# Kernel tuning notes

Measured on AMD Instinct MI355X. Metric: run time of the kernel, lower is better.

## Reference

```python
import jax, jax.numpy as jnp
import numpy as np

H = 48; W = 48; WS = 8; NH = 12; FTH = 0.4; EPS = 1e-6


def _layernorm(x, w, b):
    mu = jnp.mean(x, axis=-1, keepdims=True)
    var = jnp.mean((x - mu) ** 2, axis=-1, keepdims=True)
    return (x - mu) * jax.lax.rsqrt(var + EPS) * w + b


def _mha(x, w_qkv, b_qkv, w_o, b_o, key_mask=None):
    # x: (Bn, N, C); w_qkv: (3, C, C); key_mask: (Bn, N) bool or None
    Bn, N, C = x.shape
    d = C // NH
    qkv = jnp.einsum('bnc,tcd->tbnd', x, w_qkv) + b_qkv[:, None, None, :]
    q, k, v = [t.reshape(Bn, N, NH, d).transpose(0, 2, 1, 3) for t in qkv]
    s = jnp.einsum('bhqd,bhkd->bhqk', q, k) / jnp.sqrt(jnp.asarray(d, x.dtype))
    if key_mask is not None:
        s = jnp.where(key_mask[:, None, None, :], s, jnp.asarray(-1e9, s.dtype))
    p = jax.nn.softmax(s, axis=-1)
    ctx = jnp.einsum('bhqk,bhkd->bhqd', p, v).transpose(0, 2, 1, 3).reshape(Bn, N, C)
    return ctx @ w_o + b_o


def _forward(x, mask, w_qkv_g, b_qkv_g, w_o_g, b_o_g, w_qkv_l, b_qkv_l, w_o_l, b_o_l,
             ln1_w, ln1_b, ln2_w, ln2_b, w_fc1, b_fc1, w_fc2, b_fc2):
    B, L, C = x.shape
    shortcut = x
    xn = _layernorm(x, ln1_w, ln1_b)

    # avg_pool2d(mask, 4, 4) -> (B, H, W); fg/bg split
    pooled = mask.reshape(B, 1, H, 4, W, 4).mean(axis=(3, 5))[:, 0]      # (B,H,W)
    fg = pooled > FTH                                                    # bool (B,H,W)
    fg_tok = fg.reshape(B, L)
    bg = (~fg).astype(x.dtype)
    # window-level bg mask: avg_pool(bg, WS) > 0 -> window contains any bg token
    bg_win = bg.reshape(B, H // WS, WS, W // WS, WS).mean(axis=(2, 4)) > 0.0   # (B, nH, nW)
    bg_win_tok = jnp.broadcast_to(bg_win[:, :, None, :, None],
                                  (B, H // WS, WS, W // WS, WS)).reshape(B, L)

    # local windowed attention on all windows (equivalent on bg windows; masked out elsewhere)
    xw = xn.reshape(B, H // WS, WS, W // WS, WS, C).transpose(0, 1, 3, 2, 4, 5)
    xw = xw.reshape(-1, WS * WS, C)                                      # (B*nWin, WS*WS, C)
    lout = _mha(xw, w_qkv_l, b_qkv_l, w_o_l, b_o_l)
    lout = lout.reshape(B, H // WS, W // WS, WS, WS, C).transpose(0, 1, 3, 2, 4, 5)
    lout = lout.reshape(B, L, C)

    # global attention with fg key mask (fg queries attend fg keys only)
    gout = _mha(xn, w_qkv_g, b_qkv_g, w_o_g, b_o_g, key_mask=fg_tok)

    # scatter-back semantics: fg positions take global output; bg-window positions take local output; rest zero
    zero = jnp.zeros((), x.dtype)
    x_new = jnp.where(fg_tok[..., None], gout,
                      jnp.where(bg_win_tok[..., None], lout, zero))

    x1 = shortcut + x_new
    h = _layernorm(x1, ln2_w, ln2_b)
    h = jax.nn.gelu(h @ w_fc1 + b_fc1, approximate=False) @ w_fc2 + b_fc2
    return x1 + h


def setup_inputs() -> dict:
    key = jax.random.key(0)
    ks = jax.random.split(key, 8)
    B, L, C, M = 2, H * W, 768, 3072
    s = 0.02
    return {
        'x': jax.random.normal(ks[0], (B, L, C), jnp.float32),
        'mask': jax.random.uniform(ks[1], (B, 1, 4 * H, 4 * W), jnp.float32),
        'w_qkv_g': jax.random.normal(ks[2], (3, C, C), jnp.float32) * s,
        'b_qkv_g': jnp.zeros((3, C), jnp.float32),
        'w_o_g': jax.random.normal(ks[3], (C, C), jnp.float32) * s,
        'b_o_g': jnp.zeros((C,), jnp.float32),
        'w_qkv_l': jax.random.normal(ks[4], (3, C, C), jnp.float32) * s,
        'b_qkv_l': jnp.zeros((3, C), jnp.float32),
        'w_o_l': jax.random.normal(ks[5], (C, C), jnp.float32) * s,
        'b_o_l': jnp.zeros((C,), jnp.float32),
        'ln1_w': jnp.ones((C,), jnp.float32),
        'ln1_b': jnp.zeros((C,), jnp.float32),
        'ln2_w': jnp.ones((C,), jnp.float32),
        'ln2_b': jnp.zeros((C,), jnp.float32),
        'w_fc1': jax.random.normal(ks[6], (C, M), jnp.float32) * s,
        'b_fc1': jnp.zeros((M,), jnp.float32),
        'w_fc2': jax.random.normal(ks[7], (M, C), jnp.float32) * s,
        'b_fc2': jnp.zeros((C,), jnp.float32),
    }


def reference(x, mask, w_qkv_g, b_qkv_g, w_o_g, b_o_g, w_qkv_l, b_qkv_l, w_o_l, b_o_l,
              ln1_w, ln1_b, ln2_w, ln2_b, w_fc1, b_fc1, w_fc2, b_fc2):
    return _forward(x, mask, w_qkv_g, b_qkv_g, w_o_g, b_o_g, w_qkv_l, b_qkv_l, w_o_l, b_o_l,
                    ln1_w, ln1_b, ln2_w, ln2_b, w_fc1, b_fc1, w_fc2, b_fc2)
```

## Files before the change

kernel.cpp:

```cpp
#include <hip/hip_runtime.h>
#include <math.h>

#define Lh 2304
#define Ch 768
#define NHh 12
#define Bh 2
#define QS 4608

typedef unsigned short ushort_t;
typedef unsigned int uint_t;
typedef __attribute__((ext_vector_type(8))) short bf16x8;
typedef __attribute__((ext_vector_type(4))) float f32x4;
#define MFMA16(a, b, c) __builtin_amdgcn_mfma_f32_16x16x32_bf16(a, b, c, 0, 0, 0)

__device__ __forceinline__ ushort_t f2bf(float f) {
    union { float f; uint_t u; } v; v.f = f;
    uint_t u = v.u + 0x7fffu + ((v.u >> 16) & 1u);
    return (ushort_t)(u >> 16);
}
__device__ __forceinline__ uint_t pack2bf(float a, float b) {
    return (uint_t)f2bf(a) | ((uint_t)f2bf(b) << 16);
}

__device__ __forceinline__ void llds16(ushort_t* dst, const ushort_t* src) {
    __builtin_amdgcn_global_load_lds(
        (__attribute__((address_space(1))) void*)(const_cast<ushort_t*>(src)),
        (__attribute__((address_space(3))) void*)dst, 16, 0, 0);
}

__global__ __launch_bounds__(256)
void layernorm_bf16_kernel(const float* __restrict__ x, const float* __restrict__ w,
                           const float* __restrict__ b, ushort_t* __restrict__ y)
{
    int row = blockIdx.x;
    int tid = threadIdx.x;
    const float* xr = x + (size_t)row * Ch;
    float v0 = xr[tid], v1 = xr[tid + 256], v2 = xr[tid + 512];
    __shared__ float red[256];
    red[tid] = v0 + v1 + v2;
    __syncthreads();
    for (int st = 128; st > 0; st >>= 1) {
        if (tid < st) red[tid] += red[tid + st];
        __syncthreads();
    }
    float mean = red[0] * (1.0f / 768.0f);
    __syncthreads();
    float d0 = v0 - mean, d1 = v1 - mean, d2 = v2 - mean;
    red[tid] = d0 * d0 + d1 * d1 + d2 * d2;
    __syncthreads();
    for (int st = 128; st > 0; st >>= 1) {
        if (tid < st) red[tid] += red[tid + st];
        __syncthreads();
    }
    float rstd = rsqrtf(red[0] * (1.0f / 768.0f) + 1e-6f);
    ushort_t* yr = y + (size_t)row * Ch;
    yr[tid]       = f2bf(d0 * rstd * w[tid]       + b[tid]);
    yr[tid + 256] = f2bf(d1 * rstd * w[tid + 256] + b[tid + 256]);
    yr[tid + 512] = f2bf(d2 * rstd * w[tid + 512] + b[tid + 512]);
}

__global__ __launch_bounds__(64)
void mask_kernel(const float* __restrict__ mask, float* __restrict__ fg,
                 float* __restrict__ bgw)
{
    int win = blockIdx.x;
    int b = win / 36, w = win % 36;
    int wi = w / 6, wj = w % 6;
    int lane = threadIdx.x;
    int i = wi * 8 + (lane >> 3), j = wj * 8 + (lane & 7);
    const float* mb = mask + (size_t)b * 192 * 192 + (size_t)(i * 4) * 192 + j * 4;
    float s = 0.0f;
    #pragma unroll
    for (int di = 0; di < 4; ++di) {
        float4 v = *(const float4*)(mb + (size_t)di * 192);
        s += v.x + v.y + v.z + v.w;
    }
    float f = (s * (1.0f / 16.0f) > 0.4f) ? 1.0f : 0.0f;
    fg[b * Lh + i * 48 + j] = f;
    unsigned long long bg = __ballot(f == 0.0f);
    if (lane == 0) bgw[win] = bg ? 1.0f : 0.0f;
}

__global__ __launch_bounds__(256)
void transpose_all_kernel(const float* __restrict__ w_qkv_g, const float* __restrict__ w_qkv_l,
                          const float* __restrict__ w_o_g, const float* __restrict__ w_o_l,
                          const float* __restrict__ w_fc1, const float* __restrict__ w_fc2,
                          ushort_t* __restrict__ wtq, ushort_t* __restrict__ wt_o_g,
                          ushort_t* __restrict__ wt_o_l, ushort_t* __restrict__ wt_fc1,
                          ushort_t* __restrict__ wt_fc2)
{
    int blk = blockIdx.x;
    const float* W; ushort_t* D; int K, N, nx, bx;
    const size_t CC = (size_t)Ch * Ch;
    if (blk < 432)       { int t = blk / 144; bx = blk % 144;
                           W = w_qkv_g + t * CC; D = wtq + t * CC; K = 768; N = 768; nx = 12; }
    else if (blk < 864)  { int r = blk - 432; int t = r / 144; bx = r % 144;
                           W = w_qkv_l + t * CC; D = wtq + (size_t)2304 * 768 + t * CC;
                           K = 768; N = 768; nx = 12; }
    else if (blk < 1008) { bx = blk - 864;  W = w_o_g; D = wt_o_g; K = 768; N = 768; nx = 12; }
    else if (blk < 1152) { bx = blk - 1008; W = w_o_l; D = wt_o_l; K = 768; N = 768; nx = 12; }
    else if (blk < 1728) { bx = blk - 1152; W = w_fc1; D = wt_fc1; K = 768; N = 3072; nx = 48; }
    else                 { bx = blk - 1728; W = w_fc2; D = wt_fc2; K = 3072; N = 768; nx = 12; }
    int n0 = (bx % nx) * 64;
    int k0 = (bx / nx) * 64;
    int tid = threadIdx.x;
    __shared__ float T[64][65];
    #pragma unroll
    for (int i = 0; i < 16; ++i) {
        int lin = i * 256 + tid;
        int r = lin >> 6, c = lin & 63;
        T[r][c] = W[(size_t)(k0 + r) * N + n0 + c];
    }
    __syncthreads();
    #pragma unroll
    for (int i = 0; i < 4; ++i) {
        int lin = i * 256 + tid;
        int r = lin >> 4, c0 = (lin & 15) * 4;
        uint_t lo = pack2bf(T[c0][r], T[c0 + 1][r]);
        uint_t hi = pack2bf(T[c0 + 2][r], T[c0 + 3][r]);
        *(uint2*)&D[(size_t)(n0 + r) * K + k0 + c0] = make_uint2(lo, hi);
    }
}

template<int BNt>
__global__ __launch_bounds__(256)
void gemm_bf16_t(const ushort_t* __restrict__ A, const ushort_t* __restrict__ Bt,
                 const float* __restrict__ bias, const float* __restrict__ residual,
                 void* __restrict__ C, int M, int N, int K, int flags)
{
    __shared__ ushort_t AsL[2][128 * 32];
    __shared__ ushort_t BsL[2][BNt * 32];
    int bm = blockIdx.y * 128;
    int bn = blockIdx.x * BNt;
    int tid = threadIdx.x;
    int lane = tid & 63;
    int wave = tid >> 6;
    int wm = wave >> 1, wn = wave & 1;
    int quad = lane >> 4, l15 = lane & 15;
    constexpr int NJ = BNt / 32;

    int srow = lane >> 2;
    int sg8 = ((lane & 3) ^ ((lane >> 3) & 3)) * 8;
    int fsw = (l15 >> 1) & 3;

    f32x4 acc[4][NJ];
    #pragma unroll
    for (int i = 0; i < 4; ++i)
        #pragma unroll
        for (int j = 0; j < NJ; ++j)
            acc[i][j] = (f32x4){0.f, 0.f, 0.f, 0.f};

    int iters = K / 32;
    llds16(&AsL[0][wave * 512], A + (size_t)(bm + wave * 16 + srow) * K + sg8);
    llds16(&AsL[0][(wave + 4) * 512], A + (size_t)(bm + (wave + 4) * 16 + srow) * K + sg8);
    llds16(&BsL[0][wave * 512], Bt + (size_t)(bn + wave * 16 + srow) * K + sg8);
    if (BNt == 128)
        llds16(&BsL[0][(wave + 4) * 512], Bt + (size_t)(bn + (wave + 4) * 16 + srow) * K + sg8);

    for (int kt = 0; kt < iters; ++kt) {
        int cur = kt & 1;
        __syncthreads();

        bf16x8 af[4], bfr[NJ];
        #pragma unroll
        for (int i = 0; i < 4; ++i)
            af[i] = *(const bf16x8*)&AsL[cur][(wm * 64 + i * 16 + l15) * 32 + ((quad ^ fsw) * 8)];
        #pragma unroll
        for (int j = 0; j < NJ; ++j)
            bfr[j] = *(const bf16x8*)&BsL[cur][(wn * (BNt / 2) + j * 16 + l15) * 32 + ((quad ^ fsw) * 8)];

        if (kt + 1 < iters) {
            int k0 = (kt + 1) * 32;
            int nxt = 1 - cur;
            llds16(&AsL[nxt][wave * 512], A + (size_t)(bm + wave * 16 + srow) * K + k0 + sg8);
            llds16(&AsL[nxt][(wave + 4) * 512], A + (size_t)(bm + (wave + 4) * 16 + srow) * K + k0 + sg8);
            llds16(&BsL[nxt][wave * 512], Bt + (size_t)(bn + wave * 16 + srow) * K + k0 + sg8);
            if (BNt == 128)
                llds16(&BsL[nxt][(wave + 4) * 512], Bt + (size_t)(bn + (wave + 4) * 16 + srow) * K + k0 + sg8);
        }

        #pragma unroll
        for (int i = 0; i < 4; ++i)
            #pragma unroll
            for (int j = 0; j < NJ; ++j)
                acc[i][j] = MFMA16(bfr[j], af[i], acc[i][j]);
    }

    #pragma unroll
    for (int i = 0; i < 4; ++i) {
        int row = bm + wm * 64 + i * 16 + l15;
        #pragma unroll
        for (int j = 0; j < NJ; ++j) {
            int col = bn + wn * (BNt / 2) + j * 16 + quad * 4;
            float4 bia = *(const float4*)&bias[col];
            float o0 = acc[i][j][0] + bia.x;
            float o1 = acc[i][j][1] + bia.y;
            float o2 = acc[i][j][2] + bia.z;
            float o3 = acc[i][j][3] + bia.w;
            if (flags & 1) {
                o0 = o0 * 0.5f * (1.0f + erff(o0 * 0.70710678f));
                o1 = o1 * 0.5f * (1.0f + erff(o1 * 0.70710678f));
                o2 = o2 * 0.5f * (1.0f + erff(o2 * 0.70710678f));
                o3 = o3 * 0.5f * (1.0f + erff(o3 * 0.70710678f));
            }
            if (residual) {
                float4 rs = *(const float4*)&residual[(size_t)row * N + col];
                o0 += rs.x; o1 += rs.y; o2 += rs.z; o3 += rs.w;
            }
            if (flags & 2) {
                *(uint2*)&((ushort_t*)C)[(size_t)row * N + col] =
                    make_uint2(pack2bf(o0, o1), pack2bf(o2, o3));
            } else {
                *(float4*)&((float*)C)[(size_t)row * N + col] =
                    make_float4(o0, o1, o2, o3);
            }
        }
    }
}

__global__ __launch_bounds__(256)
void oproj_dual_kernel(const ushort_t* __restrict__ ctxg, const ushort_t* __restrict__ ctxl,
                       const ushort_t* __restrict__ Wg, const ushort_t* __restrict__ Wl,
                       const float* __restrict__ biasg, const float* __restrict__ biasl,
                       const float* __restrict__ x, float* __restrict__ x1,
                       const float* __restrict__ fg, const float* __restrict__ bgw)
{
    __shared__ ushort_t AsL[2][128 * 32];
    __shared__ ushort_t BsL[2][64 * 32];
    int bm = blockIdx.y * 128;
    int bn = blockIdx.x * 64;
    int tid = threadIdx.x;
    int lane = tid & 63;
    int wave = tid >> 6;
    int wm = wave >> 1, wn = wave & 1;
    int quad = lane >> 4, l15 = lane & 15;

    int srow = lane >> 2;
    int sg8 = ((lane & 3) ^ ((lane >> 3) & 3)) * 8;
    int fsw = (l15 >> 1) & 3;
    const int K = Ch, N = Ch, iters = Ch / 32;

    f32x4 accg[4][2], accl[4][2];
    #pragma unroll
    for (int i = 0; i < 4; ++i)
        #pragma unroll
        for (int j = 0; j < 2; ++j) {
            accg[i][j] = (f32x4){0.f, 0.f, 0.f, 0.f};
            accl[i][j] = (f32x4){0.f, 0.f, 0.f, 0.f};
        }

    #pragma unroll
    for (int pass = 0; pass < 2; ++pass) {
        const ushort_t* A = pass ? ctxl : ctxg;
        const ushort_t* Bt = pass ? Wl : Wg;
        if (pass) __syncthreads();
        llds16(&AsL[0][wave * 512], A + (size_t)(bm + wave * 16 + srow) * K + sg8);
        llds16(&AsL[0][(wave + 4) * 512], A + (size_t)(bm + (wave + 4) * 16 + srow) * K + sg8);
        llds16(&BsL[0][wave * 512], Bt + (size_t)(bn + wave * 16 + srow) * K + sg8);

        for (int kt = 0; kt < iters; ++kt) {
            int cur = kt & 1;
            __syncthreads();
            bf16x8 af[4], bfr[2];
            #pragma unroll
            for (int i = 0; i < 4; ++i)
                af[i] = *(const bf16x8*)&AsL[cur][(wm * 64 + i * 16 + l15) * 32 + ((quad ^ fsw) * 8)];
            #pragma unroll
            for (int j = 0; j < 2; ++j)
                bfr[j] = *(const bf16x8*)&BsL[cur][(wn * 32 + j * 16 + l15) * 32 + ((quad ^ fsw) * 8)];
            if (kt + 1 < iters) {
                int k0 = (kt + 1) * 32;
                int nxt = 1 - cur;
                llds16(&AsL[nxt][wave * 512], A + (size_t)(bm + wave * 16 + srow) * K + k0 + sg8);
                llds16(&AsL[nxt][(wave + 4) * 512], A + (size_t)(bm + (wave + 4) * 16 + srow) * K + k0 + sg8);
                llds16(&BsL[nxt][wave * 512], Bt + (size_t)(bn + wave * 16 + srow) * K + k0 + sg8);
            }
            if (pass == 0) {
                #pragma unroll
                for (int i = 0; i < 4; ++i)
                    #pragma unroll
                    for (int j = 0; j < 2; ++j)
                        accg[i][j] = MFMA16(bfr[j], af[i], accg[i][j]);
            } else {
                #pragma unroll
                for (int i = 0; i < 4; ++i)
                    #pragma unroll
                    for (int j = 0; j < 2; ++j)
                        accl[i][j] = MFMA16(bfr[j], af[i], accl[i][j]);
            }
        }
    }

    #pragma unroll
    for (int i = 0; i < 4; ++i) {
        int row = bm + wm * 64 + i * 16 + l15;
        int bb = (row >= Lh) ? 1 : 0;
        int n = row - bb * Lh;
        int ii = n / 48, jj = n % 48;
        float keepg = (fg[row] != 0.0f) ? 1.0f : 0.0f;
        float keepl = (keepg == 0.0f &&
                       bgw[bb * 36 + (ii >> 3) * 6 + (jj >> 3)] != 0.0f) ? 1.0f : 0.0f;
        #pragma unroll
        for (int j = 0; j < 2; ++j) {
            int col = bn + wn * 32 + j * 16 + quad * 4;
            float4 bg4 = *(const float4*)&biasg[col];
            float4 bl4 = *(const float4*)&biasl[col];
            float4 x4 = *(const float4*)&x[(size_t)row * N + col];
            float4 o;
            o.x = x4.x + keepg * (accg[i][j][0] + bg4.x) + keepl * (accl[i][j][0] + bl4.x);
            o.y = x4.y + keepg * (accg[i][j][1] + bg4.y) + keepl * (accl[i][j][1] + bl4.y);
            o.z = x4.z + keepg * (accg[i][j][2] + bg4.z) + keepl * (accl[i][j][2] + bl4.z);
            o.w = x4.w + keepg * (accg[i][j][3] + bg4.w) + keepl * (accl[i][j][3] + bl4.w);
            *(float4*)&x1[(size_t)row * N + col] = o;
        }
    }
}

__device__ __forceinline__ void attn_global_body(
    const ushort_t* __restrict__ QKV, const float* __restrict__ fg,
    ushort_t* __restrict__ O, int tile, int h, int b,
    ushort_t (*Ks)[72], ushort_t (*Vt)[72], ushort_t (*Ps)[72], float* fgs)
{
    int tid = threadIdx.x;
    int lane = tid & 63;
    int wave = tid >> 6;
    int quad = lane >> 4, l15 = lane & 15;

    bf16x8 aq[2][2];
    #pragma unroll
    for (int s = 0; s < 2; ++s) {
        int ql = wave * 32 + s * 16 + l15;
        int tok = tile * 128 + ql;
        const ushort_t* qbase = QKV + (size_t)(b * Lh + tok) * QS + h * 64;
        #pragma unroll
        for (int step = 0; step < 2; ++step)
            aq[s][step] = *(const bf16x8*)(qbase + step * 32 + quad * 8);
    }

    float l_part[2] = {0.f, 0.f};
    f32x4 o_acc[2][4];
    #pragma unroll
    for (int s = 0; s < 2; ++s)
        #pragma unroll
        for (int t4 = 0; t4 < 4; ++t4) o_acc[s][t4] = (f32x4){0.f, 0.f, 0.f, 0.f};

    uint4 kx[2], vx[2];
    #pragma unroll
    for (int it = 0; it < 2; ++it) {
        int e = tid + it * 256;
        int row = e >> 3, g = e & 7;
        const ushort_t* base = QKV + (size_t)(b * Lh + row) * QS + h * 64 + g * 8;
        kx[it] = *(const uint4*)(base + 768);
        vx[it] = *(const uint4*)(base + 1536);
    }
    float fgn = 0.f;
    if (tid < 64) fgn = fg[b * Lh + tid];

    for (int kt = 0; kt < 36; ++kt) {
        __syncthreads();
        #pragma unroll
        for (int it = 0; it < 2; ++it) {
            int e = tid + it * 256;
            int row = e >> 3, g = e & 7;
            *(uint4*)&Ks[row][g * 8] = kx[it];
            union { uint4 raw; ushort_t us[8]; } vv;
            vv.raw = vx[it];
            int col = row ^ (g << 3);
            #pragma unroll
            for (int j = 0; j < 8; ++j) Vt[g * 8 + j][col] = vv.us[j];
        }
        if (tid < 64) fgs[tid] = (fgn - 1.0f) * 1e9f;
        __syncthreads();

        if (kt + 1 < 36) {
            #pragma unroll
            for (int it = 0; it < 2; ++it) {
                int e = tid + it * 256;
                int row = e >> 3, g = e & 7;
                int tok = (kt + 1) * 64 + row;
                const ushort_t* base = QKV + (size_t)(b * Lh + tok) * QS + h * 64 + g * 8;
                kx[it] = *(const uint4*)(base + 768);
                vx[it] = *(const uint4*)(base + 1536);
            }
            if (tid < 64) fgn = fg[b * Lh + (kt + 1) * 64 + tid];
        }

        f32x4 s4[2][4];
        #pragma unroll
        for (int s = 0; s < 2; ++s)
            #pragma unroll
            for (int j4 = 0; j4 < 4; ++j4) s4[s][j4] = (f32x4){0.f, 0.f, 0.f, 0.f};
        #pragma unroll
        for (int step = 0; step < 2; ++step) {
            bf16x8 bk[4];
            #pragma unroll
            for (int j4 = 0; j4 < 4; ++j4)
                bk[j4] = *(const bf16x8*)&Ks[j4 * 16 + l15][step * 32 + quad * 8];
            #pragma unroll
            for (int s = 0; s < 2; ++s)
                #pragma unroll
                for (int j4 = 0; j4 < 4; ++j4)
                    s4[s][j4] = MFMA16(bk[j4], aq[s][step], s4[s][j4]);
        }
        #pragma unroll
        for (int s = 0; s < 2; ++s) {
            int p0 = wave * 32 + s * 16;
            #pragma unroll
            for (int j4 = 0; j4 < 4; ++j4) {
                float4 mb4 = *(const float4*)&fgs[j4 * 16 + quad * 4];
                float e0 = __expf(s4[s][j4][0] * 0.125f + mb4.x);
                float e1 = __expf(s4[s][j4][1] * 0.125f + mb4.y);
                float e2 = __expf(s4[s][j4][2] * 0.125f + mb4.z);
                float e3 = __expf(s4[s][j4][3] * 0.125f + mb4.w);
                l_part[s] += (e0 + e1) + (e2 + e3);
                uint_t a01 = __builtin_amdgcn_perm(__float_as_uint(e1), __float_as_uint(e0), 0x07060302u);
                uint_t a23 = __builtin_amdgcn_perm(__float_as_uint(e3), __float_as_uint(e2), 0x07060302u);
                *(uint2*)&Ps[p0 + l15][j4 * 16 + quad * 4] = make_uint2(a01, a23);
            }
        }
        #pragma unroll
        for (int step = 0; step < 2; ++step) {
            bf16x8 bv[4];
            #pragma unroll
            for (int t4 = 0; t4 < 4; ++t4) {
                int dd = t4 * 16 + l15;
                int cb = ((step * 4 + quad) ^ ((dd >> 3) & 7)) * 8;
                bv[t4] = *(const bf16x8*)&Vt[dd][cb];
            }
            #pragma unroll
            for (int s = 0; s < 2; ++s) {
                int p0 = wave * 32 + s * 16;
                bf16x8 a = *(const bf16x8*)&Ps[p0 + l15][step * 32 + quad * 8];
                #pragma unroll
                for (int t4 = 0; t4 < 4; ++t4)
                    o_acc[s][t4] = MFMA16(bv[t4], a, o_acc[s][t4]);
            }
        }
    }

    #pragma unroll
    for (int s = 0; s < 2; ++s) {
        float v = l_part[s];
        v += __shfl_xor(v, 16, 64);
        v += __shfl_xor(v, 32, 64);
        float inv = 1.0f / v;
        int ql = wave * 32 + s * 16 + l15;
        int tok = tile * 128 + ql;
        ushort_t* ob = O + (size_t)(b * Lh + tok) * Ch + h * 64;
        #pragma unroll
        for (int t4 = 0; t4 < 4; ++t4) {
            *(uint2*)&ob[t4 * 16 + quad * 4] =
                make_uint2(pack2bf(o_acc[s][t4][0] * inv, o_acc[s][t4][1] * inv),
                           pack2bf(o_acc[s][t4][2] * inv, o_acc[s][t4][3] * inv));
        }
    }
}

__device__ __forceinline__ void attn_local_body(
    const ushort_t* __restrict__ QKV, ushort_t* __restrict__ O,
    int tile, int h, int b,
    ushort_t (*Ks)[72], ushort_t (*Vt)[72], ushort_t (*Ps)[72])
{
    int tid = threadIdx.x;
    int lane = tid & 63;
    int wave = tid >> 6;
    int quad = lane >> 4, l15 = lane & 15;
    int wi = tile / 6, wj = tile % 6;

    bf16x8 aq[2];
    {
        int ql = wave * 16 + l15;
        int tok = (wi * 8 + (ql >> 3)) * 48 + wj * 8 + (ql & 7);
        const ushort_t* qbase = QKV + (size_t)(b * Lh + tok) * QS + 2304 + h * 64;
        #pragma unroll
        for (int step = 0; step < 2; ++step)
            aq[step] = *(const bf16x8*)(qbase + step * 32 + quad * 8);
    }

    float l_part = 0.f;
    f32x4 o_acc[4];
    #pragma unroll
    for (int t4 = 0; t4 < 4; ++t4) o_acc[t4] = (f32x4){0.f, 0.f, 0.f, 0.f};

    #pragma unroll
    for (int it = 0; it < 2; ++it) {
        int e = tid + it * 256;
        int row = e >> 3, g = e & 7;
        int tok = (wi * 8 + (row >> 3)) * 48 + wj * 8 + (row & 7);
        const ushort_t* base = QKV + (size_t)(b * Lh + tok) * QS + 2304 + h * 64 + g * 8;
        uint4 kvv = *(const uint4*)(base + 768);
        *(uint4*)&Ks[row][g * 8] = kvv;
        union { uint4 raw; ushort_t us[8]; } vv;
        vv.raw = *(const uint4*)(base + 1536);
        int col = row ^ (g << 3);
        #pragma unroll
        for (int j = 0; j < 8; ++j) Vt[g * 8 + j][col] = vv.us[j];
    }
    __syncthreads();

    f32x4 s4[4];
    #pragma unroll
    for (int j4 = 0; j4 < 4; ++j4) s4[j4] = (f32x4){0.f, 0.f, 0.f, 0.f};
    #pragma unroll
    for (int step = 0; step < 2; ++step) {
        bf16x8 bk[4];
        #pragma unroll
        for (int j4 = 0; j4 < 4; ++j4)
            bk[j4] = *(const bf16x8*)&Ks[j4 * 16 + l15][step * 32 + quad * 8];
        #pragma unroll
        for (int j4 = 0; j4 < 4; ++j4)
            s4[j4] = MFMA16(bk[j4], aq[step], s4[j4]);
    }
    int p0 = wave * 16;
    #pragma unroll
    for (int j4 = 0; j4 < 4; ++j4) {
        float e0 = __expf(s4[j4][0] * 0.125f);
        float e1 = __expf(s4[j4][1] * 0.125f);
        float e2 = __expf(s4[j4][2] * 0.125f);
        float e3 = __expf(s4[j4][3] * 0.125f);
        l_part += (e0 + e1) + (e2 + e3);
        uint_t a01 = __builtin_amdgcn_perm(__float_as_uint(e1), __float_as_uint(e0), 0x07060302u);
        uint_t a23 = __builtin_amdgcn_perm(__float_as_uint(e3), __float_as_uint(e2), 0x07060302u);
        *(uint2*)&Ps[p0 + l15][j4 * 16 + quad * 4] = make_uint2(a01, a23);
    }
    #pragma unroll
    for (int step = 0; step < 2; ++step) {
        bf16x8 bv[4];
        #pragma unroll
        for (int t4 = 0; t4 < 4; ++t4) {
            int dd = t4 * 16 + l15;
            int cb = ((step * 4 + quad) ^ ((dd >> 3) & 7)) * 8;
            bv[t4] = *(const bf16x8*)&Vt[dd][cb];
        }
        bf16x8 a = *(const bf16x8*)&Ps[p0 + l15][step * 32 + quad * 8];
        #pragma unroll
        for (int t4 = 0; t4 < 4; ++t4)
            o_acc[t4] = MFMA16(bv[t4], a, o_acc[t4]);
    }

    {
        float v = l_part;
        v += __shfl_xor(v, 16, 64);
        v += __shfl_xor(v, 32, 64);
        float inv = 1.0f / v;
        int ql = wave * 16 + l15;
        int tok = (wi * 8 + (ql >> 3)) * 48 + wj * 8 + (ql & 7);
        ushort_t* ob = O + (size_t)(b * Lh + tok) * Ch + h * 64;
        #pragma unroll
        for (int t4 = 0; t4 < 4; ++t4) {
            *(uint2*)&ob[t4 * 16 + quad * 4] =
                make_uint2(pack2bf(o_acc[t4][0] * inv, o_acc[t4][1] * inv),
                           pack2bf(o_acc[t4][2] * inv, o_acc[t4][3] * inv));
        }
    }
}

__global__ __launch_bounds__(256)
void attn_fused_kernel(const ushort_t* __restrict__ QKV, const float* __restrict__ fg,
                       ushort_t* __restrict__ ctxg, ushort_t* __restrict__ ctxl)
{
    __shared__ ushort_t Ks[64][72];
    __shared__ ushort_t Vt[64][72];
    __shared__ ushort_t Ps[128][72];
    __shared__ float fgs[64];

    int gid = blockIdx.x;
    if (gid < 432) {
        int tile = gid % 18;
        int h = (gid / 18) % NHh;
        int b = gid / (18 * NHh);
        attn_global_body(QKV, fg, ctxg, tile, h, b, Ks, Vt, Ps, fgs);
    } else {
        int rr = gid - 432;
        int tile = rr % 36;
        int h = (rr / 36) % NHh;
        int b = rr / (36 * NHh);
        attn_local_body(QKV, ctxl, tile, h, b, Ks, Vt, Ps);
    }
}

extern "C" void kernel_launch(void* const* d_in, const int* in_sizes, int n_in,
                              void* d_out, int out_size, void* d_ws, size_t ws_size,
                              hipStream_t stream)
{
    const float* x       = (const float*)d_in[0];
    const float* mask    = (const float*)d_in[1];
    const float* w_qkv_g = (const float*)d_in[2];
    const float* b_qkv_g = (const float*)d_in[3];
    const float* w_o_g   = (const float*)d_in[4];
    const float* b_o_g   = (const float*)d_in[5];
    const float* w_qkv_l = (const float*)d_in[6];
    const float* b_qkv_l = (const float*)d_in[7];
    const float* w_o_l   = (const float*)d_in[8];
    const float* b_o_l   = (const float*)d_in[9];
    const float* ln1_w   = (const float*)d_in[10];
    const float* ln1_b   = (const float*)d_in[11];
    const float* ln2_w   = (const float*)d_in[12];
    const float* ln2_b   = (const float*)d_in[13];
    const float* w_fc1   = (const float*)d_in[14];
    const float* b_fc1   = (const float*)d_in[15];
    const float* w_fc2   = (const float*)d_in[16];
    const float* b_fc2   = (const float*)d_in[17];
    float* out = (float*)d_out;

    const size_t U = (size_t)Bh * Lh * Ch;
    char* p = (char*)d_ws;
    ushort_t* qkvb = (ushort_t*)p;        p += (size_t)4608 * 4608 * 2;
    ushort_t* midb = qkvb;
    ushort_t* ctxg = (ushort_t*)p;        p += U * 2;
    ushort_t* ctxl = (ushort_t*)p;        p += U * 2;
    ushort_t* xnb  = (ushort_t*)p;        p += U * 2;
    float*    x1   = (float*)p;           p += U * 4;
    ushort_t* wtq  = (ushort_t*)p;        p += (size_t)4608 * 768 * 2;
    ushort_t* wt_o_g = (ushort_t*)p;      p += (size_t)768 * 768 * 2;
    ushort_t* wt_o_l = (ushort_t*)p;      p += (size_t)768 * 768 * 2;
    ushort_t* wt_fc1 = (ushort_t*)p;      p += (size_t)3072 * 768 * 2;
    ushort_t* wt_fc2 = (ushort_t*)p;      p += (size_t)768 * 3072 * 2;
    float*    biasq  = (float*)p;         p += 4608 * 4;
    float*    fg     = (float*)p;         p += Bh * Lh * 4;
    float*    bgw    = (float*)p;

    const int Mrows = Bh * Lh;
    dim3 blk(256);

    hipMemcpyAsync(biasq, b_qkv_g, 2304 * sizeof(float), hipMemcpyDeviceToDevice, stream);
    hipMemcpyAsync(biasq + 2304, b_qkv_l, 2304 * sizeof(float), hipMemcpyDeviceToDevice, stream);

    transpose_all_kernel<<<2304, blk, 0, stream>>>(
        w_qkv_g, w_qkv_l, w_o_g, w_o_l, w_fc1, w_fc2,
        wtq, wt_o_g, wt_o_l, wt_fc1, wt_fc2);

    layernorm_bf16_kernel<<<Mrows, blk, 0, stream>>>(x, ln1_w, ln1_b, xnb);
    mask_kernel<<<72, dim3(64), 0, stream>>>(mask, fg, bgw);

    gemm_bf16_t<128><<<dim3(4608 / 128, Mrows / 128), blk, 0, stream>>>(
        xnb, wtq, biasq, nullptr, qkvb, Mrows, 4608, Ch, 2);

    attn_fused_kernel<<<1296, blk, 0, stream>>>(qkvb, fg, ctxg, ctxl);

    oproj_dual_kernel<<<dim3(Ch / 64, Mrows / 128), blk, 0, stream>>>(
        ctxg, ctxl, wt_o_g, wt_o_l, b_o_g, b_o_l, x, x1, fg, bgw);

    layernorm_bf16_kernel<<<Mrows, blk, 0, stream>>>(x1, ln2_w, ln2_b, xnb);

    gemm_bf16_t<128><<<dim3(3072 / 128, Mrows / 128), blk, 0, stream>>>(
        xnb, wt_fc1, b_fc1, nullptr, midb, Mrows, 3072, Ch, 1 | 2);
    gemm_bf16_t<64><<<dim3(Ch / 64, Mrows / 128), blk, 0, stream>>>(
        midb, wt_fc2, b_fc2, x1, out, Mrows, Ch, 3072, 0);
}
```

Baseline: 409.0 us.

## Halve global attention query tile, remap blocks across XCDs, use exp2

Global attention blocks now handle 64 queries instead of 128, so there are twice as many blocks (864 instead of 432) and the Ps shared buffer shrinks, which should help occupancy and load balance. Block indices for both the global and local paths are permuted with an interleave of 8 so that neighbouring work lands on the same XCD for L2 reuse. Softmax exponentials switch to exp2 with a log2(e)-prescaled scale and mask constant. The trade-off is that each K/V tile loaded into shared memory now serves half as many queries, so K/V load traffic per query doubles.

Measured after the change: 429.3 us. 1.05x slower.

```diff
diff --git a/kernel.cpp b/kernel.cpp
--- a/kernel.cpp
+++ b/kernel.cpp
@@ -12,6 +12,14 @@
 typedef __attribute__((ext_vector_type(8))) short bf16x8;
 typedef __attribute__((ext_vector_type(4))) float f32x4;
 #define MFMA16(a, b, c) __builtin_amdgcn_mfma_f32_16x16x32_bf16(a, b, c, 0, 0, 0)
+
+#define SCL2 0.18033688f
+#define MSK2 1.4426950e9f
+#if __has_builtin(__builtin_amdgcn_exp2f)
+#define EXP2F(x) __builtin_amdgcn_exp2f(x)
+#else
+#define EXP2F(x) exp2f(x)
+#endif
 
 __device__ __forceinline__ ushort_t f2bf(float f) {
     union { float f; uint_t u; } v; v.f = f;
@@ -326,23 +334,20 @@
     int wave = tid >> 6;
     int quad = lane >> 4, l15 = lane & 15;
 
-    bf16x8 aq[2][2];
-    #pragma unroll
-    for (int s = 0; s < 2; ++s) {
-        int ql = wave * 32 + s * 16 + l15;
-        int tok = tile * 128 + ql;
+    int ql = wave * 16 + l15;
+    int tok = tile * 64 + ql;
+    bf16x8 aq[2];
+    {
         const ushort_t* qbase = QKV + (size_t)(b * Lh + tok) * QS + h * 64;
         #pragma unroll
         for (int step = 0; step < 2; ++step)
-            aq[s][step] = *(const bf16x8*)(qbase + step * 32 + quad * 8);
-    }
-
-    float l_part[2] = {0.f, 0.f};
-    f32x4 o_acc[2][4];
-    #pragma unroll
-    for (int s = 0; s < 2; ++s)
-        #pragma unroll
-        for (int t4 = 0; t4 < 4; ++t4) o_acc[s][t4] = (f32x4){0.f, 0.f, 0.f, 0.f};
+            aq[step] = *(const bf16x8*)(qbase + step * 32 + quad * 8);
+    }
+
+    float l_part = 0.f;
+    f32x4 o_acc[4];
+    #pragma unroll
+    for (int t4 = 0; t4 < 4; ++t4) o_acc[t4] = (f32x4){0.f, 0.f, 0.f, 0.f};
 
     uint4 kx[2], vx[2];
     #pragma unroll
@@ -369,7 +374,7 @@
             #pragma unroll
             for (int j = 0; j < 8; ++j) Vt[g * 8 + j][col] = vv.us[j];
         }
-        if (tid < 64) fgs[tid] = (fgn - 1.0f) * 1e9f;
+        if (tid < 64) fgs[tid] = (fgn - 1.0f) * MSK2;
         __syncthreads();
 
         if (kt + 1 < 36) {
@@ -377,19 +382,17 @@
             for (int it = 0; it < 2; ++it) {
                 int e = tid + it * 256;
                 int row = e >> 3, g = e & 7;
-                int tok = (kt + 1) * 64 + row;
-                const ushort_t* base = QKV + (size_t)(b * Lh + tok) * QS + h * 64 + g * 8;
+                int tok2 = (kt + 1) * 64 + row;
+                const ushort_t* base = QKV + (size_t)(b * Lh + tok2) * QS + h * 64 + g * 8;
                 kx[it] = *(const uint4*)(base + 768);
                 vx[it] = *(const uint4*)(base + 1536);
             }
             if (tid < 64) fgn = fg[b * Lh + (kt + 1) * 64 + tid];
         }
 
-        f32x4 s4[2][4];
-        #pragma unroll
-        for (int s = 0; s < 2; ++s)
-            #pragma unroll
-            for (int j4 = 0; j4 < 4; ++j4) s4[s][j4] = (f32x4){0.f, 0.f, 0.f, 0.f};
+        f32x4 s4[4];
+        #pragma unroll
+        for (int j4 = 0; j4 < 4; ++j4) s4[j4] = (f32x4){0.f, 0.f, 0.f, 0.f};
         #pragma unroll
         for (int step = 0; step < 2; ++step) {
             bf16x8 bk[4];
@@ -397,26 +400,21 @@
             for (int j4 = 0; j4 < 4; ++j4)
                 bk[j4] = *(const bf16x8*)&Ks[j4 * 16 + l15][step * 32 + quad * 8];
             #pragma unroll
-            for (int s = 0; s < 2; ++s)
-                #pragma unroll
-                for (int j4 = 0; j4 < 4; ++j4)
-                    s4[s][j4] = MFMA16(bk[j4], aq[s][step], s4[s][j4]);
-        }
-        #pragma unroll
-        for (int s = 0; s < 2; ++s) {
-            int p0 = wave * 32 + s * 16;
-            #pragma unroll
-            for (int j4 = 0; j4 < 4; ++j4) {
-                float4 mb4 = *(const float4*)&fgs[j4 * 16 + quad * 4];
-                float e0 = __expf(s4[s][j4][0] * 0.125f + mb4.x);
-                float e1 = __expf(s4[s][j4][1] * 0.125f + mb4.y);
-                float e2 = __expf(s4[s][j4][2] * 0.125f + mb4.z);
-                float e3 = __expf(s4[s][j4][3] * 0.125f + mb4.w);
-                l_part[s] += (e0 + e1) + (e2 + e3);
-                uint_t a01 = __builtin_amdgcn_perm(__float_as_uint(e1), __float_as_uint(e0), 0x07060302u);
-                uint_t a23 = __builtin_amdgcn_perm(__float_as_uint(e3), __float_as_uint(e2), 0x07060302u);
-                *(uint2*)&Ps[p0 + l15][j4 * 16 + quad * 4] = make_uint2(a01, a23);
-            }
+            for (int j4 = 0; j4 < 4; ++j4)
+                s4[j4] = MFMA16(bk[j4], aq[step], s4[j4]);
+        }
+        int p0 = wave * 16;
+        #pragma unroll
+        for (int j4 = 0; j4 < 4; ++j4) {
+            float4 mb4 = *(const float4*)&fgs[j4 * 16 + quad * 4];
+            float e0 = EXP2F(s4[j4][0] * SCL2 + mb4.x);
+            float e1 = EXP2F(s4[j4][1] * SCL2 + mb4.y);
+            float e2 = EXP2F(s4[j4][2] * SCL2 + mb4.z);
+            float e3 = EXP2F(s4[j4][3] * SCL2 + mb4.w);
+            l_part += (e0 + e1) + (e2 + e3);
+            uint_t a01 = __builtin_amdgcn_perm(__float_as_uint(e1), __float_as_uint(e0), 0x07060302u);
+            uint_t a23 = __builtin_amdgcn_perm(__float_as_uint(e3), __float_as_uint(e2), 0x07060302u);
+            *(uint2*)&Ps[p0 + l15][j4 * 16 + quad * 4] = make_uint2(a01, a23);
         }
         #pragma unroll
         for (int step = 0; step < 2; ++step) {
@@ -427,31 +425,24 @@
                 int cb = ((step * 4 + quad) ^ ((dd >> 3) & 7)) * 8;
                 bv[t4] = *(const bf16x8*)&Vt[dd][cb];
             }
-            #pragma unroll
-            for (int s = 0; s < 2; ++s) {
-                int p0 = wave * 32 + s * 16;
-                bf16x8 a = *(const bf16x8*)&Ps[p0 + l15][step * 32 + quad * 8];
-                #pragma unroll
-                for (int t4 = 0; t4 < 4; ++t4)
-                    o_acc[s][t4] = MFMA16(bv[t4], a, o_acc[s][t4]);
-            }
-        }
-    }
-
-    #pragma unroll
-    for (int s = 0; s < 2; ++s) {
-        float v = l_part[s];
+            bf16x8 a = *(const bf16x8*)&Ps[p0 + l15][step * 32 + quad * 8];
+            #pragma unroll
+            for (int t4 = 0; t4 < 4; ++t4)
+                o_acc[t4] = MFMA16(bv[t4], a, o_acc[t4]);
+        }
+    }
+
+    {
+        float v = l_part;
         v += __shfl_xor(v, 16, 64);
         v += __shfl_xor(v, 32, 64);
         float inv = 1.0f / v;
-        int ql = wave * 32 + s * 16 + l15;
-        int tok = tile * 128 + ql;
         ushort_t* ob = O + (size_t)(b * Lh + tok) * Ch + h * 64;
         #pragma unroll
         for (int t4 = 0; t4 < 4; ++t4) {
             *(uint2*)&ob[t4 * 16 + quad * 4] =
-                make_uint2(pack2bf(o_acc[s][t4][0] * inv, o_acc[s][t4][1] * inv),
-                           pack2bf(o_acc[s][t4][2] * inv, o_acc[s][t4][3] * inv));
+                make_uint2(pack2bf(o_acc[t4][0] * inv, o_acc[t4][1] * inv),
+                           pack2bf(o_acc[t4][2] * inv, o_acc[t4][3] * inv));
         }
     }
 }
@@ -514,10 +505,10 @@
     int p0 = wave * 16;
     #pragma unroll
     for (int j4 = 0; j4 < 4; ++j4) {
-        float e0 = __expf(s4[j4][0] * 0.125f);
-        float e1 = __expf(s4[j4][1] * 0.125f);
-        float e2 = __expf(s4[j4][2] * 0.125f);
-        float e3 = __expf(s4[j4][3] * 0.125f);
+        float e0 = EXP2F(s4[j4][0] * SCL2);
+        float e1 = EXP2F(s4[j4][1] * SCL2);
+        float e2 = EXP2F(s4[j4][2] * SCL2);
+        float e3 = EXP2F(s4[j4][3] * SCL2);
         l_part += (e0 + e1) + (e2 + e3);
         uint_t a01 = __builtin_amdgcn_perm(__float_as_uint(e1), __float_as_uint(e0), 0x07060302u);
         uint_t a23 = __builtin_amdgcn_perm(__float_as_uint(e3), __float_as_uint(e2), 0x07060302u);
@@ -561,20 +552,22 @@
 {
     __shared__ ushort_t Ks[64][72];
     __shared__ ushort_t Vt[64][72];
-    __shared__ ushort_t Ps[128][72];
+    __shared__ ushort_t Ps[64][72];
     __shared__ float fgs[64];
 
-    int gid = blockIdx.x;
-    if (gid < 432) {
-        int tile = gid % 18;
-        int h = (gid / 18) % NHh;
-        int b = gid / (18 * NHh);
+    int bid = blockIdx.x;
+    if (bid < 864) {
+        int gid = (bid & 7) * 108 + (bid >> 3);
+        int tile = gid % 36;
+        int h = (gid / 36) % NHh;
+        int b = gid / 432;
         attn_global_body(QKV, fg, ctxg, tile, h, b, Ks, Vt, Ps, fgs);
     } else {
-        int rr = gid - 432;
-        int tile = rr % 36;
-        int h = (rr / 36) % NHh;
-        int b = rr / (36 * NHh);
+        int rr = bid - 864;
+        int lid = (rr & 7) * 108 + (rr >> 3);
+        int tile = lid % 36;
+        int h = (lid / 36) % NHh;
+        int b = lid / 432;
         attn_local_body(QKV, ctxl, tile, h, b, Ks, Vt, Ps);
     }
 }
@@ -636,7 +629,7 @@
     gemm_bf16_t<128><<<dim3(4608 / 128, Mrows / 128), blk, 0, stream>>>(
         xnb, wtq, biasq, nullptr, qkvb, Mrows, 4608, Ch, 2);
 
-    attn_fused_kernel<<<1296, blk, 0, stream>>>(qkvb, fg, ctxg, ctxl);
+    attn_fused_kernel<<<1728, blk, 0, stream>>>(qkvb, fg, ctxg, ctxl);
 
     oproj_dual_kernel<<<dim3(Ch / 64, Mrows / 128), blk, 0, stream>>>(
         ctxg, ctxl, wt_o_g, wt_o_l, b_o_g, b_o_l, x, x1, fg, bgw);
```

## Split global attention keys in halves with a merge kernel, use exp2

Applied to the files above, without the earlier changes.

Global attention now splits the key range into two halves, doubling the block count. Each half writes unnormalised fp32 partial outputs and row sums, and a new merge kernel combines them into the bf16 context. Softmax uses exp2 with a pre-scaled log2e factor, and block indices are remapped with an interleaved stride. This adds fp32 partial-buffer traffic and an extra kernel launch in exchange for more parallelism and a longer block tail. The x1 buffer is aliased to the partial buffer, which is safe only because the merge runs before the output projection.

Measured after the change: 410.0 us. Within noise of the previous version (+0.2%).

```diff
diff --git a/kernel.cpp b/kernel.cpp
--- a/kernel.cpp
+++ b/kernel.cpp
@@ -12,6 +12,14 @@
 typedef __attribute__((ext_vector_type(8))) short bf16x8;
 typedef __attribute__((ext_vector_type(4))) float f32x4;
 #define MFMA16(a, b, c) __builtin_amdgcn_mfma_f32_16x16x32_bf16(a, b, c, 0, 0, 0)
+
+#define SCL2 0.18033688f
+#define MSK2 1.4426950e9f
+#if __has_builtin(__builtin_amdgcn_exp2f)
+#define EXP2F(x) __builtin_amdgcn_exp2f(x)
+#else
+#define EXP2F(x) exp2f(x)
+#endif
 
 __device__ __forceinline__ ushort_t f2bf(float f) {
     union { float f; uint_t u; } v; v.f = f;
@@ -318,13 +326,15 @@
 
 __device__ __forceinline__ void attn_global_body(
     const ushort_t* __restrict__ QKV, const float* __restrict__ fg,
-    ushort_t* __restrict__ O, int tile, int h, int b,
+    float* __restrict__ Opart, float* __restrict__ Lpart,
+    int tile, int h, int b, int half,
     ushort_t (*Ks)[72], ushort_t (*Vt)[72], ushort_t (*Ps)[72], float* fgs)
 {
     int tid = threadIdx.x;
     int lane = tid & 63;
     int wave = tid >> 6;
     int quad = lane >> 4, l15 = lane & 15;
+    int kb0 = half * 1152;
 
     bf16x8 aq[2][2];
     #pragma unroll
@@ -349,14 +359,14 @@
     for (int it = 0; it < 2; ++it) {
         int e = tid + it * 256;
         int row = e >> 3, g = e & 7;
-        const ushort_t* base = QKV + (size_t)(b * Lh + row) * QS + h * 64 + g * 8;
+        const ushort_t* base = QKV + (size_t)(b * Lh + kb0 + row) * QS + h * 64 + g * 8;
         kx[it] = *(const uint4*)(base + 768);
         vx[it] = *(const uint4*)(base + 1536);
     }
     float fgn = 0.f;
-    if (tid < 64) fgn = fg[b * Lh + tid];
-
-    for (int kt = 0; kt < 36; ++kt) {
+    if (tid < 64) fgn = fg[b * Lh + kb0 + tid];
+
+    for (int kt = 0; kt < 18; ++kt) {
         __syncthreads();
         #pragma unroll
         for (int it = 0; it < 2; ++it) {
@@ -369,20 +379,20 @@
             #pragma unroll
             for (int j = 0; j < 8; ++j) Vt[g * 8 + j][col] = vv.us[j];
         }
-        if (tid < 64) fgs[tid] = (fgn - 1.0f) * 1e9f;
+        if (tid < 64) fgs[tid] = (fgn - 1.0f) * MSK2;
         __syncthreads();
 
-        if (kt + 1 < 36) {
+        if (kt + 1 < 18) {
             #pragma unroll
             for (int it = 0; it < 2; ++it) {
                 int e = tid + it * 256;
                 int row = e >> 3, g = e & 7;
-                int tok = (kt + 1) * 64 + row;
-                const ushort_t* base = QKV + (size_t)(b * Lh + tok) * QS + h * 64 + g * 8;
+                int tok2 = kb0 + (kt + 1) * 64 + row;
+                const ushort_t* base = QKV + (size_t)(b * Lh + tok2) * QS + h * 64 + g * 8;
                 kx[it] = *(const uint4*)(base + 768);
                 vx[it] = *(const uint4*)(base + 1536);
             }
-            if (tid < 64) fgn = fg[b * Lh + (kt + 1) * 64 + tid];
+            if (tid < 64) fgn = fg[b * Lh + kb0 + (kt + 1) * 64 + tid];
         }
 
         f32x4 s4[2][4];
@@ -408,10 +418,10 @@
             #pragma unroll
             for (int j4 = 0; j4 < 4; ++j4) {
                 float4 mb4 = *(const float4*)&fgs[j4 * 16 + quad * 4];
-                float e0 = __expf(s4[s][j4][0] * 0.125f + mb4.x);
-                float e1 = __expf(s4[s][j4][1] * 0.125f + mb4.y);
-                float e2 = __expf(s4[s][j4][2] * 0.125f + mb4.z);
-                float e3 = __expf(s4[s][j4][3] * 0.125f + mb4.w);
+                float e0 = EXP2F(s4[s][j4][0] * SCL2 + mb4.x);
+                float e1 = EXP2F(s4[s][j4][1] * SCL2 + mb4.y);
+                float e2 = EXP2F(s4[s][j4][2] * SCL2 + mb4.z);
+                float e3 = EXP2F(s4[s][j4][3] * SCL2 + mb4.w);
                 l_part[s] += (e0 + e1) + (e2 + e3);
                 uint_t a01 = __builtin_amdgcn_perm(__float_as_uint(e1), __float_as_uint(e0), 0x07060302u);
                 uint_t a23 = __builtin_amdgcn_perm(__float_as_uint(e3), __float_as_uint(e2), 0x07060302u);
@@ -443,16 +453,14 @@
         float v = l_part[s];
         v += __shfl_xor(v, 16, 64);
         v += __shfl_xor(v, 32, 64);
-        float inv = 1.0f / v;
         int ql = wave * 32 + s * 16 + l15;
         int tok = tile * 128 + ql;
-        ushort_t* ob = O + (size_t)(b * Lh + tok) * Ch + h * 64;
-        #pragma unroll
-        for (int t4 = 0; t4 < 4; ++t4) {
-            *(uint2*)&ob[t4 * 16 + quad * 4] =
-                make_uint2(pack2bf(o_acc[s][t4][0] * inv, o_acc[s][t4][1] * inv),
-                           pack2bf(o_acc[s][t4][2] * inv, o_acc[s][t4][3] * inv));
-        }
+        float* op = Opart + ((size_t)half * 4608 + b * Lh + tok) * Ch + h * 64;
+        #pragma unroll
+        for (int t4 = 0; t4 < 4; ++t4)
+            *(f32x4*)&op[t4 * 16 + quad * 4] = o_acc[s][t4];
+        if (quad == 0)
+            Lpart[((size_t)half * 4608 + b * Lh + tok) * NHh + h] = v;
     }
 }
 
@@ -514,10 +522,10 @@
     int p0 = wave * 16;
     #pragma unroll
     for (int j4 = 0; j4 < 4; ++j4) {
-        float e0 = __expf(s4[j4][0] * 0.125f);
-        float e1 = __expf(s4[j4][1] * 0.125f);
-        float e2 = __expf(s4[j4][2] * 0.125f);
-        float e3 = __expf(s4[j4][3] * 0.125f);
+        float e0 = EXP2F(s4[j4][0] * SCL2);
+        float e1 = EXP2F(s4[j4][1] * SCL2);
+        float e2 = EXP2F(s4[j4][2] * SCL2);
+        float e3 = EXP2F(s4[j4][3] * SCL2);
         l_part += (e0 + e1) + (e2 + e3);
         uint_t a01 = __builtin_amdgcn_perm(__float_as_uint(e1), __float_as_uint(e0), 0x07060302u);
         uint_t a23 = __builtin_amdgcn_perm(__float_as_uint(e3), __float_as_uint(e2), 0x07060302u);
@@ -557,26 +565,51 @@
 
 __global__ __launch_bounds__(256)
 void attn_fused_kernel(const ushort_t* __restrict__ QKV, const float* __restrict__ fg,
-                       ushort_t* __restrict__ ctxg, ushort_t* __restrict__ ctxl)
+                       float* __restrict__ Opart, float* __restrict__ Lpart,
+                       ushort_t* __restrict__ ctxl)
 {
     __shared__ ushort_t Ks[64][72];
     __shared__ ushort_t Vt[64][72];
     __shared__ ushort_t Ps[128][72];
     __shared__ float fgs[64];
 
-    int gid = blockIdx.x;
-    if (gid < 432) {
-        int tile = gid % 18;
-        int h = (gid / 18) % NHh;
-        int b = gid / (18 * NHh);
-        attn_global_body(QKV, fg, ctxg, tile, h, b, Ks, Vt, Ps, fgs);
+    int bid = blockIdx.x;
+    if (bid < 864) {
+        int gid = (bid & 7) * 108 + (bid >> 3);
+        int half = gid / 432;
+        int rem = gid % 432;
+        int tile = rem % 18;
+        int h = (rem / 18) % NHh;
+        int b = rem / 216;
+        attn_global_body(QKV, fg, Opart, Lpart, tile, h, b, half, Ks, Vt, Ps, fgs);
     } else {
-        int rr = gid - 432;
-        int tile = rr % 36;
-        int h = (rr / 36) % NHh;
-        int b = rr / (36 * NHh);
+        int rr = bid - 864;
+        int lid = (rr & 7) * 108 + (rr >> 3);
+        int tile = lid % 36;
+        int h = (lid / 36) % NHh;
+        int b = lid / 432;
         attn_local_body(QKV, ctxl, tile, h, b, Ks, Vt, Ps);
     }
+}
+
+__global__ __launch_bounds__(192)
+void attn_merge_kernel(const float* __restrict__ Op, const float* __restrict__ Lp,
+                       ushort_t* __restrict__ ctxg)
+{
+    int r = blockIdx.x;
+    int tid = threadIdx.x;
+    int d = tid * 4;
+    int h = d >> 6;
+    float la = Lp[(size_t)r * NHh + h];
+    float lb = Lp[((size_t)4608 + r) * NHh + h];
+    float inv = 1.0f / (la + lb);
+    const float* pa = Op + (size_t)r * Ch + d;
+    const float* pb = Op + (size_t)4608 * Ch + (size_t)r * Ch + d;
+    float4 a = *(const float4*)pa;
+    float4 b4 = *(const float4*)pb;
+    *(uint2*)&ctxg[(size_t)r * Ch + d] =
+        make_uint2(pack2bf((a.x + b4.x) * inv, (a.y + b4.y) * inv),
+                   pack2bf((a.z + b4.z) * inv, (a.w + b4.w) * inv));
 }
 
 extern "C" void kernel_launch(void* const* d_in, const int* in_sizes, int n_in,
@@ -610,7 +643,9 @@
     ushort_t* ctxg = (ushort_t*)p;        p += U * 2;
     ushort_t* ctxl = (ushort_t*)p;        p += U * 2;
     ushort_t* xnb  = (ushort_t*)p;        p += U * 2;
-    float*    x1   = (float*)p;           p += U * 4;
+    float*    Opart = (float*)p;          p += (size_t)2 * U * 4;
+    float*    Lpart = (float*)p;          p += (size_t)2 * 4608 * NHh * 4;
+    float*    x1   = Opart;
     ushort_t* wtq  = (ushort_t*)p;        p += (size_t)4608 * 768 * 2;
     ushort_t* wt_o_g = (ushort_t*)p;      p += (size_t)768 * 768 * 2;
     ushort_t* wt_o_l = (ushort_t*)p;      p += (size_t)768 * 768 * 2;
@@ -636,7 +671,8 @@
     gemm_bf16_t<128><<<dim3(4608 / 128, Mrows / 128), blk, 0, stream>>>(
         xnb, wtq, biasq, nullptr, qkvb, Mrows, 4608, Ch, 2);
 
-    attn_fused_kernel<<<1296, blk, 0, stream>>>(qkvb, fg, ctxg, ctxl);
+    attn_fused_kernel<<<1728, blk, 0, stream>>>(qkvb, fg, Opart, Lpart, ctxl);
+    attn_merge_kernel<<<Mrows, dim3(192), 0, stream>>>(Opart, Lpart, ctxg);
 
     oproj_dual_kernel<<<dim3(Ch / 64, Mrows / 128), blk, 0, stream>>>(
         ctxg, ctxl, wt_o_g, wt_o_l, b_o_g, b_o_l, x, x1, fg, bgw);
```
